# Kernel optimization log

Hardware: AMD Instinct MI355X
Metric: run time of the kernel (lower is better)

The kernel has to match this reference:

```python
import jax, jax.numpy as jnp
import numpy as np

DN = ('NCHW', 'OIHW', 'NCHW')

def conv2d(x, w, b):
    y = jax.lax.conv_general_dilated(x, w, (1, 1), 'SAME', dimension_numbers=DN)
    return y + b[None, :, None, None]

def deform_conv2d(x, offset, w, b):
    # torchvision DeformConv2d v1: kernel 3x3, stride 1, pad 1, dilation 1, no mask.
    # offset: [B, 18, H, W] ordered (dy0, dx0, dy1, dx1, ...) over row-major kernel taps.
    B, C, H, W = x.shape
    K2 = 9
    ki = (jnp.arange(K2) // 3).astype(x.dtype)  # kernel row index i
    kj = (jnp.arange(K2) % 3).astype(x.dtype)   # kernel col index j
    dy = offset[:, 0::2]  # [B, 9, H, W]
    dx = offset[:, 1::2]
    hh = jnp.arange(H, dtype=x.dtype)
    ww = jnp.arange(W, dtype=x.dtype)
    # sampling positions: p = out_pos - pad + k + offset
    py = hh[None, None, :, None] + ki[None, :, None, None] - 1.0 + dy  # [B,9,H,W]
    px = ww[None, None, None, :] + kj[None, :, None, None] - 1.0 + dx

    xf = x.reshape(B, C, H * W)
    y0 = jnp.floor(py); x0 = jnp.floor(px)
    y1 = y0 + 1.0;      x1 = x0 + 1.0
    wy1 = py - y0; wy0 = 1.0 - wy1
    wx1 = px - x0; wx0 = 1.0 - wx1

    def corner(yc, xc, cw):
        valid = (yc >= 0) & (yc <= H - 1) & (xc >= 0) & (xc <= W - 1)
        yi = jnp.clip(yc, 0, H - 1).astype(jnp.int32)
        xi = jnp.clip(xc, 0, W - 1).astype(jnp.int32)
        idx = yi * W + xi                       # [B,9,H,W]
        v = jax.vmap(lambda img, i: img[:, i])(xf, idx)  # [B,C,9,H,W]
        return v * (cw * valid.astype(x.dtype))[:, None]

    sampled = (corner(y0, x0, wy0 * wx0) + corner(y0, x1, wy0 * wx1)
               + corner(y1, x0, wy1 * wx0) + corner(y1, x1, wy1 * wx1))  # [B,C,9,H,W]
    out = jnp.einsum('bckhw,ock->bohw', sampled, w.reshape(w.shape[0], C, K2))
    return out + b[None, :, None, None]

def setup_inputs() -> dict:
    key = jax.random.key(0)
    ks = jax.random.split(key, 20)
    B, C, H, W = 8, 64, 128, 128
    O = 64
    s = 0.05
    inp = {
        'x': jax.random.normal(ks[0], (B, C, H, W), jnp.float32),
        'bsize': jax.random.uniform(ks[1], (B, 2), jnp.float32),
        # glob: Linear(2,64) -> ReLU -> Linear(64,32)
        'gw1': s * jax.random.normal(ks[2], (64, 2), jnp.float32),
        'gb1': jnp.zeros((64,), jnp.float32),
        'gw2': s * jax.random.normal(ks[3], (32, 64), jnp.float32),
        'gb2': jnp.zeros((32,), jnp.float32),
        # local: Conv2d(C,32,3) -> ReLU -> Conv2d(32,32,3)
        'lw1': s * jax.random.normal(ks[4], (32, C, 3, 3), jnp.float32),
        'lb1': jnp.zeros((32,), jnp.float32),
        'lw2': s * jax.random.normal(ks[5], (32, 32, 3, 3), jnp.float32),
        'lb2': jnp.zeros((32,), jnp.float32),
        # fuse: Conv2d(64,32,3) -> ReLU -> Conv2d(32,18,3)
        'fw1': s * jax.random.normal(ks[6], (32, 64, 3, 3), jnp.float32),
        'fb1': jnp.zeros((32,), jnp.float32),
        'fw2': s * jax.random.normal(ks[7], (18, 32, 3, 3), jnp.float32),
        'fb2': jnp.zeros((18,), jnp.float32),
        # deformable conv weight (copied from the source nn.Conv2d) + its own bias
        'dw': s * jax.random.normal(ks[8], (O, C, 3, 3), jnp.float32),
        'db': jnp.zeros((O,), jnp.float32),
    }
    return inp

def reference(x, bsize, gw1, gb1, gw2, gb2, lw1, lb1, lw2, lb2,
              fw1, fb1, fw2, fb2, dw, db):
    B, C, H, W = x.shape
    # global branch: MLP on box-size -> broadcast over spatial dims
    g = jax.nn.relu(bsize @ gw1.T + gb1) @ gw2.T + gb2          # [B,32]
    g_offset = jnp.broadcast_to(g[:, :, None, None], (B, 32, H, W))
    # local branch
    l_offset = conv2d(jax.nn.relu(conv2d(x, lw1, lb1)), lw2, lb2)  # [B,32,H,W]
    # fuse -> 18 offset channels
    fused = jnp.concatenate((g_offset, l_offset), axis=1)          # [B,64,H,W]
    offset = conv2d(jax.nn.relu(conv2d(fused, fw1, fb1)), fw2, fb2)  # [B,18,H,W]
    fea = deform_conv2d(x, offset, dw, db)
    return jax.nn.relu(fea)
```

## Files before the change

### kernel.cpp

```cpp
#include <hip/hip_runtime.h>

#define BB 8
#define CC 64
#define HH 128
#define WW 128
#define HWSZ (HH*WW)

typedef _Float16 h16;
typedef __attribute__((ext_vector_type(8))) _Float16 h16x8;
typedef __attribute__((ext_vector_type(4))) _Float16 h16x4;
typedef __attribute__((ext_vector_type(2))) _Float16 h16x2;
typedef __attribute__((ext_vector_type(4))) float f32x4;

__device__ __forceinline__ void conv_pack(int j, int NCG, const float* w,
                                          int maxo, h16* dst) {
  int e = j & 7, l4 = (j >> 3) & 3, l15 = (j >> 5) & 15, f = (j >> 9) & 1;
  int cg = (j >> 10) & (NCG - 1), kt = (j >> 10) / NCG;
  int o = f * 16 + l15, c = cg * 32 + l4 * 8 + e;
  int CINw = NCG * 32;
  dst[j] = (o < maxo) ? (h16)w[(o * CINw + c) * 9 + kt] : (h16)0.f;
}

__global__ __launch_bounds__(256) void prep_kernel(
    const float* __restrict__ bsize, const float* __restrict__ gw1,
    const float* __restrict__ gb1, const float* __restrict__ gw2,
    const float* __restrict__ gb2, float* __restrict__ g,
    const float* __restrict__ lw1, const float* __restrict__ lw2,
    const float* __restrict__ fw1, const float* __restrict__ fw2,
    const float* __restrict__ dw, h16* __restrict__ cwq,
    h16* __restrict__ dwq, const float* __restrict__ x,
    h16* __restrict__ xt) {
  __shared__ float hbuf[BB][64];
  const int blk = blockIdx.x;
  const int tid = threadIdx.x;
  if (blk == 0) {
#pragma unroll
    for (int i2 = 0; i2 < 2; ++i2) {
      int idx = i2 * 256 + tid;
      int b = idx >> 6, i = idx & 63;
      float v = fmaf(bsize[b * 2 + 0], gw1[i * 2 + 0],
                     fmaf(bsize[b * 2 + 1], gw1[i * 2 + 1], gb1[i]));
      hbuf[b][i] = fmaxf(v, 0.f);
    }
    __syncthreads();
    int b = tid >> 5, j = tid & 31;
    float acc = gb2[j];
#pragma unroll
    for (int i = 0; i < 64; ++i) acc = fmaf(hbuf[b][i], gw2[j * 64 + i], acc);
    g[b * 32 + j] = acc;
  } else if (blk <= 360) {
    int i = (blk - 1) * 256 + tid;
    if (i < 18432) {
      conv_pack(i, 2, lw1, 32, cwq);
    } else if (i < 27648) {
      conv_pack(i - 18432, 1, lw2, 32, cwq + 18432);
    } else if (i < 46080) {
      conv_pack(i - 27648, 2, fw1, 32, cwq + 27648);
    } else if (i < 55296) {
      conv_pack(i - 46080, 1, fw2, 18, cwq + 46080);
    } else if (i < 55296 + 36864) {
      int j = i - 55296;
      int e = j & 7, l4 = (j >> 3) & 3, l15 = (j >> 5) & 15;
      int og = (j >> 9) & 3, cg = (j >> 11) & 1, kt = j >> 12;
      int o = og * 16 + l15, c = cg * 32 + l4 * 8 + e;
      dwq[j] = (h16)dw[(o * 64 + c) * 9 + kt];
    }
  } else {
    int j = blk - 361;
    int b = (1 + j) & 7;
    int slot = j >> 3;
    int t = b * 16384 + slot * 256 + tid;
    int p = t & 16383;
    const float* xb = x + (size_t)b * 64 * HWSZ + p;
    h16* ob = xt + (size_t)t * 64;
#pragma unroll
    for (int c0 = 0; c0 < 64; c0 += 8) {
      h16x8 v;
#pragma unroll
      for (int i = 0; i < 8; ++i) v[i] = (h16)xb[(size_t)(c0 + i) * HWSZ];
      *(h16x8*)(ob + c0) = v;
    }
  }
}

template <int NCG, bool GFUSE, bool RELU, int OMODE>
__global__ __launch_bounds__(256) void conv_mfma_kernel(
    const h16* __restrict__ in, const h16* __restrict__ cwq,
    const float* __restrict__ bias, const float* __restrict__ g,
    h16* __restrict__ outv) {
  constexpr int CINS = GFUSE ? 32 : NCG * 32;
  constexpr int NS = CINS / 8;
  constexpr int LOG2NS = (NS == 8) ? 3 : 2;
  __shared__ __align__(16) h16 sh[3 * 128 * CINS];
  const int wgid = (blockIdx.x & 7) * 128 + (blockIdx.x >> 3);
  const int b = wgid >> 7, h = wgid & 127;
  const int lane = threadIdx.x & 63, wave = threadIdx.x >> 6;
  const int l15 = lane & 15, l4 = lane >> 4;
  const h16* inb = in + (size_t)b * HWSZ * CINS;

  for (int q = threadIdx.x; q < 3 * 128 * NS; q += 256) {
    int s = q & (NS - 1), pr = q >> LOG2NS;
    int r = pr >> 7, px = pr & 127;
    int gy = min(max(h - 1 + r, 0), HH - 1);
    h16x8 v = *(const h16x8*)(inb + ((size_t)gy * WW + px) * CINS + s * 8);
    *(h16x8*)(sh + pr * CINS + ((s ^ (px & (NS - 1))) * 8)) = v;
  }

  const h16x8 zfr = {0, 0, 0, 0, 0, 0, 0, 0};
  h16x8 gfr = zfr;
  if (GFUSE) {
#pragma unroll
    for (int i = 0; i < 8; ++i) gfr[i] = (h16)g[b * 32 + l4 * 8 + i];
  }
  __syncthreads();

  f32x4 acc[2][2];
#pragma unroll
  for (int f = 0; f < 2; ++f)
#pragma unroll
    for (int j = 0; j < 2; ++j) acc[f][j] = (f32x4){0.f, 0.f, 0.f, 0.f};

#pragma unroll
  for (int kt = 0; kt < 9; ++kt) {
    const int ki = kt / 3 - 1, kj = kt % 3 - 1;
    const int y = h + ki;
    const bool yok = (unsigned)y < HH;
    const int r = ki + 1;
    int xs[2];
    bool ok[2];
#pragma unroll
    for (int j = 0; j < 2; ++j) {
      int xx = wave * 32 + j * 16 + l15 + kj;
      ok[j] = yok && ((unsigned)xx < WW);
      xs[j] = min(max(xx, 0), WW - 1);
    }
#pragma unroll
    for (int cg = 0; cg < NCG; ++cg) {
      const h16* aq = cwq + (size_t)((kt * NCG + cg) * 2) * 512 + l15 * 32 + l4 * 8;
      h16x8 afr0 = *(const h16x8*)(aq);
      h16x8 afr1 = *(const h16x8*)(aq + 512);
#pragma unroll
      for (int j = 0; j < 2; ++j) {
        h16x8 bv;
        if (GFUSE && cg == 0) {
          bv = ok[j] ? gfr : zfr;
        } else {
          const int s = (!GFUSE && NCG == 2) ? cg * 4 + l4 : l4;
          h16x8 ld = *(const h16x8*)(sh + (r * 128 + xs[j]) * CINS +
                                     ((s ^ (xs[j] & (NS - 1))) * 8));
          bv = ok[j] ? ld : zfr;
        }
        acc[0][j] = __builtin_amdgcn_mfma_f32_16x16x32_f16(afr0, bv, acc[0][j], 0, 0, 0);
        acc[1][j] = __builtin_amdgcn_mfma_f32_16x16x32_f16(afr1, bv, acc[1][j], 0, 0, 0);
      }
    }
  }
  if (OMODE == 0) {
    h16* ob = outv + (size_t)b * HWSZ * 32;
#pragma unroll
    for (int f = 0; f < 2; ++f)
#pragma unroll
      for (int j = 0; j < 2; ++j) {
        int p = h * WW + wave * 32 + j * 16 + l15;
        int o0 = f * 16 + l4 * 4;
        h16x4 st;
#pragma unroll
        for (int r2 = 0; r2 < 4; ++r2) {
          float v = acc[f][j][r2] + bias[o0 + r2];
          if (RELU) v = fmaxf(v, 0.f);
          st[r2] = (h16)v;
        }
        *(h16x4*)(ob + (size_t)p * 32 + o0) = st;
      }
  } else {
    h16* ob = outv + (size_t)b * HWSZ * 24;
#pragma unroll
    for (int j = 0; j < 2; ++j) {
      int p = h * WW + wave * 32 + j * 16 + l15;
      {
        int o0 = l4 * 4;
        h16x4 st;
#pragma unroll
        for (int r2 = 0; r2 < 4; ++r2) st[r2] = (h16)(acc[0][j][r2] + bias[o0 + r2]);
        *(h16x4*)(ob + (size_t)p * 24 + o0) = st;
      }
      if (l4 == 0) {
        h16x2 st2;
        st2[0] = (h16)(acc[1][j][0] + bias[16]);
        st2[1] = (h16)(acc[1][j][1] + bias[17]);
        *(h16x2*)(ob + (size_t)p * 24 + 16) = st2;
      }
    }
  }
}

__global__ __launch_bounds__(256) void deform_mfma_kernel(
    const h16* __restrict__ xt, const h16* __restrict__ offc,
    const h16* __restrict__ dwq, const float* __restrict__ db,
    float* __restrict__ out) {
  __shared__ __align__(16) h16 sh[5 * 72 * 64];
  const int wgid = (blockIdx.x & 7) * 256 + (blockIdx.x >> 3);
  const int b = wgid >> 8;
  const int rh = wgid & 255;
  const int h = rh >> 1;
  const int halfx = (rh & 1) * 64;
  const int x_lo = halfx - 4;
  const int lane = threadIdx.x & 63, wave = threadIdx.x >> 6;
  const int l15 = lane & 15, l4 = lane >> 4;
  const int wx = halfx + wave * 16;
  const int p0 = h * WW + wx;
  const int myw = wx + l15;
  const int mypix = p0 + l15;
  const h16* xb = xt + (size_t)b * HWSZ * 64;

#pragma unroll
  for (int it = 0; it < 12; ++it) {
    int q = it * 256 + threadIdx.x;
    if (q < 2880) {
      int s = q & 7, pr = q >> 3;
      int r = pr / 72, i = pr - r * 72;
      int gy = min(max(h - 2 + r, 0), HH - 1);
      int gx = min(max(x_lo + i, 0), WW - 1);
      h16x8 v = *(const h16x8*)(xb + ((size_t)gy * WW + gx) * 64 + s * 8);
      *(h16x8*)(sh + pr * 64 + ((s ^ (i & 7)) * 8)) = v;
    }
  }

  const h16* offp = offc + ((size_t)b * HWSZ + mypix) * 24;
  h16x8 offv0 = *(const h16x8*)(offp);
  h16x8 offv1 = *(const h16x8*)(offp + 8);
  h16x8 offv2 = *(const h16x8*)(offp + 16);
  __syncthreads();

#define OFFE(e) ((e) < 8 ? (float)offv0[(e) & 7] : (e) < 16 ? (float)offv1[(e) & 7] : (float)offv2[(e) & 7])

  f32x4 acc[4];
#pragma unroll
  for (int og = 0; og < 4; ++og) acc[og] = (f32x4){0.f, 0.f, 0.f, 0.f};

  h16x8 pc[2][2][4];
  h16x8 pw[2][8];
  h16   pg[2][4];

#define PREF(kt, par) do {                                                  \
    float py = (float)(h + (kt) / 3 - 1) + OFFE(2 * (kt));                  \
    float px = (float)(myw + (kt) % 3 - 1) + OFFE(2 * (kt) + 1);            \
    float y0f = floorf(py), x0f = floorf(px);                               \
    float wy1 = py - y0f, wy0 = 1.f - wy1;                                  \
    float wx1 = px - x0f, wx0 = 1.f - wx1;                                  \
    int y0 = (int)y0f, x0i = (int)x0f;                                      \
    int y1 = y0 + 1, x1i = x0i + 1;                                         \
    bool y0ok = (unsigned)y0 < HH, y1ok = (unsigned)y1 < HH;                \
    bool x0ok = (unsigned)x0i < WW, x1ok = (unsigned)x1i < WW;              \
    pg[par][0] = (h16)((y0ok && x0ok) ? wy0 * wx0 : 0.f);                   \
    pg[par][1] = (h16)((y0ok && x1ok) ? wy0 * wx1 : 0.f);                   \
    pg[par][2] = (h16)((y1ok && x0ok) ? wy1 * wx0 : 0.f);                   \
    pg[par][3] = (h16)((y1ok && x1ok) ? wy1 * wx1 : 0.f);                   \
    int y0c = min(max(y0, 0), HH - 1), y1c = min(max(y1, 0), HH - 1);       \
    int x0c = min(max(x0i, 0), WW - 1), x1c = min(max(x1i, 0), WW - 1);     \
    int ty0u = y0c - (h - 2), ty1u = y1c - (h - 2);                         \
    int tx0u = x0c - x_lo, tx1u = x1c - x_lo;                               \
    bool fast = ((unsigned)ty0u <= 4u) & ((unsigned)ty1u <= 4u) &           \
                ((unsigned)tx0u <= 71u) & ((unsigned)tx1u <= 71u);          \
    int ty0 = min(max(ty0u, 0), 4), ty1 = min(max(ty1u, 0), 4);             \
    int tx0 = min(max(tx0u, 0), 71), tx1 = min(max(tx1u, 0), 71);           \
    int pr00 = (ty0 * 72 + tx0) * 64, pr01 = (ty0 * 72 + tx1) * 64;         \
    int pr10 = (ty1 * 72 + tx0) * 64, pr11 = (ty1 * 72 + tx1) * 64;         \
    int sx0 = (tx0 & 7) * 8, sx1 = (tx1 & 7) * 8;                           \
    _Pragma("unroll")                                                       \
    for (int cg = 0; cg < 2; ++cg) {                                        \
      int sb = (cg * 4 + l4) * 8;                                           \
      pc[par][cg][0] = *(const h16x8*)(sh + pr00 + (sb ^ sx0));             \
      pc[par][cg][1] = *(const h16x8*)(sh + pr01 + (sb ^ sx1));             \
      pc[par][cg][2] = *(const h16x8*)(sh + pr10 + (sb ^ sx0));             \
      pc[par][cg][3] = *(const h16x8*)(sh + pr11 + (sb ^ sx1));             \
    }                                                                       \
    if (!fast) {                                                            \
      int i00 = y0c * WW + x0c, i01 = y0c * WW + x1c;                       \
      int i10 = y1c * WW + x0c, i11 = y1c * WW + x1c;                       \
      _Pragma("unroll")                                                     \
      for (int cg = 0; cg < 2; ++cg) {                                      \
        const h16* cb = xb + cg * 32 + l4 * 8;                              \
        pc[par][cg][0] = *(const h16x8*)(cb + (size_t)i00 * 64);            \
        pc[par][cg][1] = *(const h16x8*)(cb + (size_t)i01 * 64);            \
        pc[par][cg][2] = *(const h16x8*)(cb + (size_t)i10 * 64);            \
        pc[par][cg][3] = *(const h16x8*)(cb + (size_t)i11 * 64);            \
      }                                                                     \
    }                                                                       \
    const h16* wq0 = dwq + ((size_t)((kt) * 2 + 0) * 64 + l15) * 32 + l4 * 8; \
    const h16* wq1 = dwq + ((size_t)((kt) * 2 + 1) * 64 + l15) * 32 + l4 * 8; \
    pw[par][0] = *(const h16x8*)(wq0 + 0 * 512);                            \
    pw[par][1] = *(const h16x8*)(wq0 + 1 * 512);                            \
    pw[par][2] = *(const h16x8*)(wq0 + 2 * 512);                            \
    pw[par][3] = *(const h16x8*)(wq0 + 3 * 512);                            \
    pw[par][4] = *(const h16x8*)(wq1 + 0 * 512);                            \
    pw[par][5] = *(const h16x8*)(wq1 + 1 * 512);                            \
    pw[par][6] = *(const h16x8*)(wq1 + 2 * 512);                            \
    pw[par][7] = *(const h16x8*)(wq1 + 3 * 512);                            \
  } while (0)

#define CONS(par) do {                                                      \
    h16 w00 = pg[par][0], w01 = pg[par][1], w10 = pg[par][2], w11 = pg[par][3]; \
    h16x8 s0 = pc[par][0][0] * w00 + pc[par][0][1] * w01                    \
             + pc[par][0][2] * w10 + pc[par][0][3] * w11;                   \
    h16x8 s1 = pc[par][1][0] * w00 + pc[par][1][1] * w01                    \
             + pc[par][1][2] * w10 + pc[par][1][3] * w11;                   \
    acc[0] = __builtin_amdgcn_mfma_f32_16x16x32_f16(s0, pw[par][0], acc[0], 0, 0, 0); \
    acc[1] = __builtin_amdgcn_mfma_f32_16x16x32_f16(s0, pw[par][1], acc[1], 0, 0, 0); \
    acc[2] = __builtin_amdgcn_mfma_f32_16x16x32_f16(s0, pw[par][2], acc[2], 0, 0, 0); \
    acc[3] = __builtin_amdgcn_mfma_f32_16x16x32_f16(s0, pw[par][3], acc[3], 0, 0, 0); \
    acc[0] = __builtin_amdgcn_mfma_f32_16x16x32_f16(s1, pw[par][4], acc[0], 0, 0, 0); \
    acc[1] = __builtin_amdgcn_mfma_f32_16x16x32_f16(s1, pw[par][5], acc[1], 0, 0, 0); \
    acc[2] = __builtin_amdgcn_mfma_f32_16x16x32_f16(s1, pw[par][6], acc[2], 0, 0, 0); \
    acc[3] = __builtin_amdgcn_mfma_f32_16x16x32_f16(s1, pw[par][7], acc[3], 0, 0, 0); \
  } while (0)

  PREF(0, 0);
  PREF(1, 1);
  CONS(0);
  PREF(2, 0);
  CONS(1);
  PREF(3, 1);
  CONS(0);
  PREF(4, 0);
  CONS(1);
  PREF(5, 1);
  CONS(0);
  PREF(6, 0);
  CONS(1);
  PREF(7, 1);
  CONS(0);
  PREF(8, 0);
  CONS(1);
  CONS(0);
#undef PREF
#undef CONS
#undef OFFE

  __syncthreads();
  float* shf = (float*)sh;
#pragma unroll
  for (int og = 0; og < 4; ++og) {
    int o = og * 16 + l15;
    float bv = db[o];
    f32x4 st;
#pragma unroll
    for (int r = 0; r < 4; ++r) st[r] = fmaxf(acc[og][r] + bv, 0.f);
    *(f32x4*)(shf + o * 68 + wave * 16 + l4 * 4) = st;
  }
  __syncthreads();
  float* outb = out + (size_t)b * CC * HWSZ + h * WW + halfx;
#pragma unroll
  for (int it2 = 0; it2 < 4; ++it2) {
    int o = wave * 16 + it2 * 4 + (lane >> 4);
    int px4 = (lane & 15) * 4;
    f32x4 v = *(const f32x4*)(shf + o * 68 + px4);
    *(f32x4*)(outb + (size_t)o * HWSZ + px4) = v;
  }
}

extern "C" void kernel_launch(void* const* d_in, const int* in_sizes, int n_in,
                              void* d_out, int out_size, void* d_ws, size_t ws_size,
                              hipStream_t stream) {
  const float* x     = (const float*)d_in[0];
  const float* bsize = (const float*)d_in[1];
  const float* gw1   = (const float*)d_in[2];
  const float* gb1   = (const float*)d_in[3];
  const float* gw2   = (const float*)d_in[4];
  const float* gb2   = (const float*)d_in[5];
  const float* lw1   = (const float*)d_in[6];
  const float* lb1   = (const float*)d_in[7];
  const float* lw2   = (const float*)d_in[8];
  const float* lb2   = (const float*)d_in[9];
  const float* fw1   = (const float*)d_in[10];
  const float* fb1   = (const float*)d_in[11];
  const float* fw2   = (const float*)d_in[12];
  const float* fb2   = (const float*)d_in[13];
  const float* dw    = (const float*)d_in[14];
  const float* db    = (const float*)d_in[15];
  float* out = (float*)d_out;

  float* gbuf = (float*)d_ws;
  h16* xt   = (h16*)((char*)d_ws + 2048);
  h16* offc = (h16*)((char*)d_ws + 2048 + (size_t)BB * HWSZ * 64 * 2);
  h16* dwq  = (h16*)((char*)offc + (size_t)BB * HWSZ * 24 * 2);

  h16* loff = (h16*)d_out;
  h16* cwq  = (h16*)d_out + 4194304;
  h16* t12  = (h16*)d_out + 8388608;
  const h16* lw1q = cwq;
  const h16* lw2q = cwq + 18432;
  const h16* fw1q = cwq + 27648;
  const h16* fw2q = cwq + 46080;

  prep_kernel<<<873, 256, 0, stream>>>(bsize, gw1, gb1, gw2, gb2, gbuf,
                                       lw1, lw2, fw1, fw2, dw, cwq, dwq, x, xt);
  conv_mfma_kernel<2, false, true, 0><<<1024, 256, 0, stream>>>(
      xt, lw1q, lb1, nullptr, t12);
  conv_mfma_kernel<1, false, false, 0><<<1024, 256, 0, stream>>>(
      t12, lw2q, lb2, nullptr, loff);
  conv_mfma_kernel<2, true, true, 0><<<1024, 256, 0, stream>>>(
      loff, fw1q, fb1, gbuf, t12);
  conv_mfma_kernel<1, false, false, 1><<<1024, 256, 0, stream>>>(
      t12, fw2q, fb2, nullptr, offc);
  deform_mfma_kernel<<<2048, 256, 0, stream>>>(xt, offc, dwq, db, out);
}
```

Baseline: 111.0 us.

## Process two output rows per workgroup to share halo rows in LDS

Each conv and deform workgroup now covers two output rows with 512 threads (8 waves) instead of one row with 256. The shared-memory tile grows from 3 to 4 rows for the convs and from 5 to 6 for deform, so the halo rows overlapping between neighbouring output rows are loaded once instead of twice. This cuts global-to-LDS traffic per output row. The cost is larger LDS use, bigger workgroups and half as many blocks, which may reduce occupancy or latency hiding.

Result: faster. 108.0 us (-2.7%).

```diff
diff --git a/kernel.cpp b/kernel.cpp
--- a/kernel.cpp
+++ b/kernel.cpp
@@ -84,24 +84,27 @@
 }
 
 template <int NCG, bool GFUSE, bool RELU, int OMODE>
-__global__ __launch_bounds__(256) void conv_mfma_kernel(
+__global__ __launch_bounds__(512) void conv_mfma_kernel(
     const h16* __restrict__ in, const h16* __restrict__ cwq,
     const float* __restrict__ bias, const float* __restrict__ g,
     h16* __restrict__ outv) {
   constexpr int CINS = GFUSE ? 32 : NCG * 32;
   constexpr int NS = CINS / 8;
   constexpr int LOG2NS = (NS == 8) ? 3 : 2;
-  __shared__ __align__(16) h16 sh[3 * 128 * CINS];
-  const int wgid = (blockIdx.x & 7) * 128 + (blockIdx.x >> 3);
-  const int b = wgid >> 7, h = wgid & 127;
+  __shared__ __align__(16) h16 sh[4 * 128 * CINS];
+  const int wgid = (blockIdx.x & 7) * 64 + (blockIdx.x >> 3);
+  const int b = wgid >> 6;
+  const int h0 = (wgid & 63) * 2;
   const int lane = threadIdx.x & 63, wave = threadIdx.x >> 6;
+  const int wr = wave >> 2, wv = wave & 3;
+  const int h = h0 + wr;
   const int l15 = lane & 15, l4 = lane >> 4;
   const h16* inb = in + (size_t)b * HWSZ * CINS;
 
-  for (int q = threadIdx.x; q < 3 * 128 * NS; q += 256) {
+  for (int q = threadIdx.x; q < 4 * 128 * NS; q += 512) {
     int s = q & (NS - 1), pr = q >> LOG2NS;
     int r = pr >> 7, px = pr & 127;
-    int gy = min(max(h - 1 + r, 0), HH - 1);
+    int gy = min(max(h0 - 1 + r, 0), HH - 1);
     h16x8 v = *(const h16x8*)(inb + ((size_t)gy * WW + px) * CINS + s * 8);
     *(h16x8*)(sh + pr * CINS + ((s ^ (px & (NS - 1))) * 8)) = v;
   }
@@ -125,12 +128,12 @@
     const int ki = kt / 3 - 1, kj = kt % 3 - 1;
     const int y = h + ki;
     const bool yok = (unsigned)y < HH;
-    const int r = ki + 1;
+    const int r = ki + 1 + wr;
     int xs[2];
     bool ok[2];
 #pragma unroll
     for (int j = 0; j < 2; ++j) {
-      int xx = wave * 32 + j * 16 + l15 + kj;
+      int xx = wv * 32 + j * 16 + l15 + kj;
       ok[j] = yok && ((unsigned)xx < WW);
       xs[j] = min(max(xx, 0), WW - 1);
     }
@@ -161,7 +164,7 @@
     for (int f = 0; f < 2; ++f)
 #pragma unroll
       for (int j = 0; j < 2; ++j) {
-        int p = h * WW + wave * 32 + j * 16 + l15;
+        int p = h * WW + wv * 32 + j * 16 + l15;
         int o0 = f * 16 + l4 * 4;
         h16x4 st;
 #pragma unroll
@@ -176,7 +179,7 @@
     h16* ob = outv + (size_t)b * HWSZ * 24;
 #pragma unroll
     for (int j = 0; j < 2; ++j) {
-      int p = h * WW + wave * 32 + j * 16 + l15;
+      int p = h * WW + wv * 32 + j * 16 + l15;
       {
         int o0 = l4 * 4;
         h16x4 st;
@@ -194,32 +197,34 @@
   }
 }
 
-__global__ __launch_bounds__(256) void deform_mfma_kernel(
+__global__ __launch_bounds__(512) void deform_mfma_kernel(
     const h16* __restrict__ xt, const h16* __restrict__ offc,
     const h16* __restrict__ dwq, const float* __restrict__ db,
     float* __restrict__ out) {
-  __shared__ __align__(16) h16 sh[5 * 72 * 64];
-  const int wgid = (blockIdx.x & 7) * 256 + (blockIdx.x >> 3);
-  const int b = wgid >> 8;
-  const int rh = wgid & 255;
-  const int h = rh >> 1;
+  __shared__ __align__(16) h16 sh[6 * 72 * 64];
+  const int wgid = (blockIdx.x & 7) * 128 + (blockIdx.x >> 3);
+  const int b = wgid >> 7;
+  const int rh = wgid & 127;
+  const int h0 = (rh >> 1) * 2;
   const int halfx = (rh & 1) * 64;
   const int x_lo = halfx - 4;
   const int lane = threadIdx.x & 63, wave = threadIdx.x >> 6;
+  const int wr = wave >> 2, wv = wave & 3;
+  const int hrow = h0 + wr;
   const int l15 = lane & 15, l4 = lane >> 4;
-  const int wx = halfx + wave * 16;
-  const int p0 = h * WW + wx;
+  const int wx = halfx + wv * 16;
+  const int p0 = hrow * WW + wx;
   const int myw = wx + l15;
   const int mypix = p0 + l15;
   const h16* xb = xt + (size_t)b * HWSZ * 64;
 
 #pragma unroll
-  for (int it = 0; it < 12; ++it) {
-    int q = it * 256 + threadIdx.x;
-    if (q < 2880) {
+  for (int it = 0; it < 7; ++it) {
+    int q = it * 512 + threadIdx.x;
+    if (q < 3456) {
       int s = q & 7, pr = q >> 3;
       int r = pr / 72, i = pr - r * 72;
-      int gy = min(max(h - 2 + r, 0), HH - 1);
+      int gy = min(max(h0 - 2 + r, 0), HH - 1);
       int gx = min(max(x_lo + i, 0), WW - 1);
       h16x8 v = *(const h16x8*)(xb + ((size_t)gy * WW + gx) * 64 + s * 8);
       *(h16x8*)(sh + pr * 64 + ((s ^ (i & 7)) * 8)) = v;
@@ -243,7 +248,7 @@
   h16   pg[2][4];
 
 #define PREF(kt, par) do {                                                  \
-    float py = (float)(h + (kt) / 3 - 1) + OFFE(2 * (kt));                  \
+    float py = (float)(hrow + (kt) / 3 - 1) + OFFE(2 * (kt));               \
     float px = (float)(myw + (kt) % 3 - 1) + OFFE(2 * (kt) + 1);            \
     float y0f = floorf(py), x0f = floorf(px);                               \
     float wy1 = py - y0f, wy0 = 1.f - wy1;                                  \
@@ -258,11 +263,11 @@
     pg[par][3] = (h16)((y1ok && x1ok) ? wy1 * wx1 : 0.f);                   \
     int y0c = min(max(y0, 0), HH - 1), y1c = min(max(y1, 0), HH - 1);       \
     int x0c = min(max(x0i, 0), WW - 1), x1c = min(max(x1i, 0), WW - 1);     \
-    int ty0u = y0c - (h - 2), ty1u = y1c - (h - 2);                         \
+    int ty0u = y0c - (h0 - 2), ty1u = y1c - (h0 - 2);                       \
     int tx0u = x0c - x_lo, tx1u = x1c - x_lo;                               \
-    bool fast = ((unsigned)ty0u <= 4u) & ((unsigned)ty1u <= 4u) &           \
+    bool fast = ((unsigned)ty0u <= 5u) & ((unsigned)ty1u <= 5u) &           \
                 ((unsigned)tx0u <= 71u) & ((unsigned)tx1u <= 71u);          \
-    int ty0 = min(max(ty0u, 0), 4), ty1 = min(max(ty1u, 0), 4);             \
+    int ty0 = min(max(ty0u, 0), 5), ty1 = min(max(ty1u, 0), 5);             \
     int tx0 = min(max(tx0u, 0), 71), tx1 = min(max(tx1u, 0), 71);           \
     int pr00 = (ty0 * 72 + tx0) * 64, pr01 = (ty0 * 72 + tx1) * 64;         \
     int pr10 = (ty1 * 72 + tx0) * 64, pr11 = (ty1 * 72 + tx1) * 64;         \
@@ -338,7 +343,7 @@
 #undef OFFE
 
   __syncthreads();
-  float* shf = (float*)sh;
+  float* shf = (float*)sh + wr * (64 * 68);
 #pragma unroll
   for (int og = 0; og < 4; ++og) {
     int o = og * 16 + l15;
@@ -346,13 +351,13 @@
     f32x4 st;
 #pragma unroll
     for (int r = 0; r < 4; ++r) st[r] = fmaxf(acc[og][r] + bv, 0.f);
-    *(f32x4*)(shf + o * 68 + wave * 16 + l4 * 4) = st;
+    *(f32x4*)(shf + o * 68 + wv * 16 + l4 * 4) = st;
   }
   __syncthreads();
-  float* outb = out + (size_t)b * CC * HWSZ + h * WW + halfx;
+  float* outb = out + (size_t)b * CC * HWSZ + hrow * WW + halfx;
 #pragma unroll
   for (int it2 = 0; it2 < 4; ++it2) {
-    int o = wave * 16 + it2 * 4 + (lane >> 4);
+    int o = wv * 16 + it2 * 4 + (lane >> 4);
     int px4 = (lane & 15) * 4;
     f32x4 v = *(const f32x4*)(shf + o * 68 + px4);
     *(f32x4*)(outb + (size_t)o * HWSZ + px4) = v;
@@ -395,13 +400,13 @@
 
   prep_kernel<<<873, 256, 0, stream>>>(bsize, gw1, gb1, gw2, gb2, gbuf,
                                        lw1, lw2, fw1, fw2, dw, cwq, dwq, x, xt);
-  conv_mfma_kernel<2, false, true, 0><<<1024, 256, 0, stream>>>(
+  conv_mfma_kernel<2, false, true, 0><<<512, 512, 0, stream>>>(
       xt, lw1q, lb1, nullptr, t12);
-  conv_mfma_kernel<1, false, false, 0><<<1024, 256, 0, stream>>>(
+  conv_mfma_kernel<1, false, false, 0><<<512, 512, 0, stream>>>(
       t12, lw2q, lb2, nullptr, loff);
-  conv_mfma_kernel<2, true, true, 0><<<1024, 256, 0, stream>>>(
+  conv_mfma_kernel<2, true, true, 0><<<512, 512, 0, stream>>>(
       loff, fw1q, fb1, gbuf, t12);
-  conv_mfma_kernel<1, false, false, 1><<<1024, 256, 0, stream>>>(
+  conv_mfma_kernel<1, false, false, 1><<<512, 512, 0, stream>>>(
       t12, fw2q, fb2, nullptr, offc);
-  deform_mfma_kernel<<<2048, 256, 0, stream>>>(xt, offc, dwq, db, out);
+  deform_mfma_kernel<<<1024, 512, 0, stream>>>(xt, offc, dwq, db, out);
 }
```

## Use direct global-to-LDS loads, two-row conv blocks, and direct deform output stores

Applied to the files above, without the earlier changes.

Global-to-shared staging in the conv and deform kernels now uses the global_load_lds builtin, with the XOR swizzle moved onto the source address. This avoids the round trip through registers. The conv kernels now use 512-thread blocks that each compute two output rows from a shared 4-row halo, which cuts redundant halo loads. The deform epilogue drops its LDS transpose and the two barriers around it, and writes 16-byte vectors straight to global memory. The trade-offs are less coalesced output writes, more LDS per conv block (lower occupancy), and reliance on the gfx950 direct-to-LDS path being waited on correctly before the barrier.

Measured after the change: 102.1 us, median of 2. 1.09x faster.

```diff
diff --git a/kernel.cpp b/kernel.cpp
--- a/kernel.cpp
+++ b/kernel.cpp
@@ -11,6 +11,9 @@
 typedef __attribute__((ext_vector_type(4))) _Float16 h16x4;
 typedef __attribute__((ext_vector_type(2))) _Float16 h16x2;
 typedef __attribute__((ext_vector_type(4))) float f32x4;
+
+typedef const __attribute__((address_space(1))) unsigned int* gptr_t;
+typedef __attribute__((address_space(3))) unsigned int* lptr_t;
 
 __device__ __forceinline__ void conv_pack(int j, int NCG, const float* w,
                                           int maxo, h16* dst) {
@@ -84,26 +87,34 @@
 }
 
 template <int NCG, bool GFUSE, bool RELU, int OMODE>
-__global__ __launch_bounds__(256) void conv_mfma_kernel(
+__global__ __launch_bounds__(512) void conv_mfma_kernel(
     const h16* __restrict__ in, const h16* __restrict__ cwq,
     const float* __restrict__ bias, const float* __restrict__ g,
     h16* __restrict__ outv) {
   constexpr int CINS = GFUSE ? 32 : NCG * 32;
   constexpr int NS = CINS / 8;
   constexpr int LOG2NS = (NS == 8) ? 3 : 2;
-  __shared__ __align__(16) h16 sh[3 * 128 * CINS];
-  const int wgid = (blockIdx.x & 7) * 128 + (blockIdx.x >> 3);
-  const int b = wgid >> 7, h = wgid & 127;
+  constexpr int NCHUNK = 4 * 128 * NS;
+  __shared__ __align__(16) h16 sh[4 * 128 * CINS];
+  const int wgid = (blockIdx.x & 7) * 64 + (blockIdx.x >> 3);
+  const int b = wgid >> 6;
+  const int h0 = (wgid & 63) * 2;
   const int lane = threadIdx.x & 63, wave = threadIdx.x >> 6;
+  const int wr = wave >> 2, wv = wave & 3;
+  const int h = h0 + wr;
   const int l15 = lane & 15, l4 = lane >> 4;
   const h16* inb = in + (size_t)b * HWSZ * CINS;
 
-  for (int q = threadIdx.x; q < 3 * 128 * NS; q += 256) {
-    int s = q & (NS - 1), pr = q >> LOG2NS;
+#pragma unroll
+  for (int it = 0; it < NCHUNK / 512; ++it) {
+    int q = it * 512 + threadIdx.x;
+    int sp = q & (NS - 1), pr = q >> LOG2NS;
     int r = pr >> 7, px = pr & 127;
-    int gy = min(max(h - 1 + r, 0), HH - 1);
-    h16x8 v = *(const h16x8*)(inb + ((size_t)gy * WW + px) * CINS + s * 8);
-    *(h16x8*)(sh + pr * CINS + ((s ^ (px & (NS - 1))) * 8)) = v;
+    int gy = min(max(h0 - 1 + r, 0), HH - 1);
+    int s = sp ^ (px & (NS - 1));
+    const h16* src = inb + ((size_t)gy * WW + px) * CINS + s * 8;
+    __builtin_amdgcn_global_load_lds(
+        (gptr_t)src, (lptr_t)(sh + (size_t)(it * 512 + wave * 64) * 8), 16, 0, 0);
   }
 
   const h16x8 zfr = {0, 0, 0, 0, 0, 0, 0, 0};
@@ -125,12 +136,12 @@
     const int ki = kt / 3 - 1, kj = kt % 3 - 1;
     const int y = h + ki;
     const bool yok = (unsigned)y < HH;
-    const int r = ki + 1;
+    const int r = ki + 1 + wr;
     int xs[2];
     bool ok[2];
 #pragma unroll
     for (int j = 0; j < 2; ++j) {
-      int xx = wave * 32 + j * 16 + l15 + kj;
+      int xx = wv * 32 + j * 16 + l15 + kj;
       ok[j] = yok && ((unsigned)xx < WW);
       xs[j] = min(max(xx, 0), WW - 1);
     }
@@ -161,7 +172,7 @@
     for (int f = 0; f < 2; ++f)
 #pragma unroll
       for (int j = 0; j < 2; ++j) {
-        int p = h * WW + wave * 32 + j * 16 + l15;
+        int p = h * WW + wv * 32 + j * 16 + l15;
         int o0 = f * 16 + l4 * 4;
         h16x4 st;
 #pragma unroll
@@ -176,7 +187,7 @@
     h16* ob = outv + (size_t)b * HWSZ * 24;
 #pragma unroll
     for (int j = 0; j < 2; ++j) {
-      int p = h * WW + wave * 32 + j * 16 + l15;
+      int p = h * WW + wv * 32 + j * 16 + l15;
       {
         int o0 = l4 * 4;
         h16x4 st;
@@ -217,12 +228,14 @@
   for (int it = 0; it < 12; ++it) {
     int q = it * 256 + threadIdx.x;
     if (q < 2880) {
-      int s = q & 7, pr = q >> 3;
+      int sp = q & 7, pr = q >> 3;
       int r = pr / 72, i = pr - r * 72;
       int gy = min(max(h - 2 + r, 0), HH - 1);
       int gx = min(max(x_lo + i, 0), WW - 1);
-      h16x8 v = *(const h16x8*)(xb + ((size_t)gy * WW + gx) * 64 + s * 8);
-      *(h16x8*)(sh + pr * 64 + ((s ^ (i & 7)) * 8)) = v;
+      int s = sp ^ (i & 7);
+      const h16* src = xb + ((size_t)gy * WW + gx) * 64 + s * 8;
+      __builtin_amdgcn_global_load_lds(
+          (gptr_t)src, (lptr_t)(sh + (size_t)(it * 256 + wave * 64) * 8), 16, 0, 0);
     }
   }
 
@@ -337,8 +350,7 @@
 #undef CONS
 #undef OFFE
 
-  __syncthreads();
-  float* shf = (float*)sh;
+  float* outb = out + (size_t)b * CC * HWSZ;
 #pragma unroll
   for (int og = 0; og < 4; ++og) {
     int o = og * 16 + l15;
@@ -346,16 +358,7 @@
     f32x4 st;
 #pragma unroll
     for (int r = 0; r < 4; ++r) st[r] = fmaxf(acc[og][r] + bv, 0.f);
-    *(f32x4*)(shf + o * 68 + wave * 16 + l4 * 4) = st;
-  }
-  __syncthreads();
-  float* outb = out + (size_t)b * CC * HWSZ + h * WW + halfx;
-#pragma unroll
-  for (int it2 = 0; it2 < 4; ++it2) {
-    int o = wave * 16 + it2 * 4 + (lane >> 4);
-    int px4 = (lane & 15) * 4;
-    f32x4 v = *(const f32x4*)(shf + o * 68 + px4);
-    *(f32x4*)(outb + (size_t)o * HWSZ + px4) = v;
+    *(f32x4*)(outb + (size_t)o * HWSZ + p0 + l4 * 4) = st;
   }
 }
 
@@ -395,13 +398,13 @@
 
   prep_kernel<<<873, 256, 0, stream>>>(bsize, gw1, gb1, gw2, gb2, gbuf,
                                        lw1, lw2, fw1, fw2, dw, cwq, dwq, x, xt);
-  conv_mfma_kernel<2, false, true, 0><<<1024, 256, 0, stream>>>(
+  conv_mfma_kernel<2, false, true, 0><<<512, 512, 0, stream>>>(
       xt, lw1q, lb1, nullptr, t12);
-  conv_mfma_kernel<1, false, false, 0><<<1024, 256, 0, stream>>>(
+  conv_mfma_kernel<1, false, false, 0><<<512, 512, 0, stream>>>(
       t12, lw2q, lb2, nullptr, loff);
-  conv_mfma_kernel<2, true, true, 0><<<1024, 256, 0, stream>>>(
+  conv_mfma_kernel<2, true, true, 0><<<512, 512, 0, stream>>>(
       loff, fw1q, fb1, gbuf, t12);
-  conv_mfma_kernel<1, false, false, 1><<<1024, 256, 0, stream>>>(
+  conv_mfma_kernel<1, false, false, 1><<<512, 512, 0, stream>>>(
       t12, fw2q, fb2, nullptr, offc);
   deform_mfma_kernel<<<2048, 256, 0, stream>>>(xt, offc, dwq, db, out);
 }
```
